# Performance work log

Measured on AMD Instinct MI355X. Metric: run time of the kernel, lower is better.

The kernel has to match this reference:

```python
import jax, jax.numpy as jnp
import numpy as np

B, C, H, W = 8, 3, 512, 512
EPS = 2e-4
N_ITER = 10  # n_iter_max default in TvChambolleDenoiser.forward


def setup_inputs() -> dict:
    key = jax.random.key(0)
    k1, k2 = jax.random.split(key)
    image = jax.random.normal(k1, (B, C, H, W), dtype=jnp.float32)
    # per-image denoising strength, typical TV weights
    weight = jax.random.uniform(k2, (B,), dtype=jnp.float32, minval=0.05, maxval=0.15)
    return {"image": image, "weight": weight}


def _denoise_tv_2d(img, w, eps=EPS, n_iter=N_ITER):
    """Chambolle TV denoising of a single 2D image (faithful to the torch loop)."""
    tau = 0.25  # 1 / (2 * ndim), ndim = 2
    numel = img.shape[0] * img.shape[1]

    def body(carry, i):
        pt, out, E_init, E_prev, done = carry
        # divergence of dual variable pt: dt = -pt.sum(0); dt[1:,:] += pt[0,:-1,:]; dt[:,1:] += pt[1,:,:-1]
        dt = -(pt[0] + pt[1])
        dt = dt.at[1:, :].add(pt[0, :-1, :])
        dt = dt.at[:, 1:].add(pt[1, :, :-1])
        out_new = jnp.where(i > 0, img + dt, img)
        Et = jnp.where(i > 0, jnp.sum(dt * dt), jnp.float32(0.0))
        # forward finite differences, zero-padded at the far boundary (gt stays 0 there)
        g0 = jnp.pad(out_new[1:, :] - out_new[:-1, :], ((0, 1), (0, 0)))
        g1 = jnp.pad(out_new[:, 1:] - out_new[:, :-1], ((0, 0), (0, 1)))
        s = g0 * g0 + g1 * g1
        # safe sqrt (forward value identical; avoids NaN grads at exact zeros)
        norm = jnp.sqrt(jnp.where(s > 0, s, 1.0)) * (s > 0)
        Et = (Et + w * jnp.sum(norm)) / numel
        gt = jnp.stack([g0, g1])  # [2, H, W]
        pt_new = (pt - tau * gt) / (1.0 + (tau / w) * norm)[None]
        E_init_new = jnp.where(i == 0, Et, E_init)
        converged = (i > 0) & (jnp.abs(E_prev - Et) < eps * E_init_new)
        # once converged (break in the torch loop), freeze all state
        pt = jnp.where(done, pt, pt_new)
        out = jnp.where(done, out, out_new)
        E_prev = jnp.where(done, E_prev, Et)
        E_init = jnp.where(done, E_init, E_init_new)
        done = done | converged
        return (pt, out, E_init, E_prev, done), None

    carry0 = (
        jnp.zeros((2,) + img.shape, img.dtype),  # pt
        img,                                      # out
        jnp.float32(0.0),                         # E_init
        jnp.float32(0.0),                         # E_previous
        jnp.bool_(False),                         # done
    )
    (pt, out, E_init, E_prev, done), _ = jax.lax.scan(body, carry0, jnp.arange(n_iter))
    return out


def reference(image, weight):
    b, c, h, w = image.shape
    imgs = image.reshape(b * c, h, w)          # each (batch, channel) slice denoised independently
    ws = jnp.repeat(weight, c)                 # per-batch weight shared across channels
    out = jax.vmap(_denoise_tv_2d)(imgs, ws)
    return out.reshape(b, c, h, w)
```

## Files before the change

kernel.cpp:

```cpp
#include <hip/hip_runtime.h>
#include <hip/hip_fp16.h>
#include <math.h>
#include <stdint.h>

#define HH 512
#define WW 512
#define NIMG 24
#define CCH 3
#define TAU 0.25f
#define TVEPS 2e-4f
#define NUMEL 262144.0f
#define NITER 10


__device__ __forceinline__ float2 h2f(uint32_t v) {
    __half2 h; *reinterpret_cast<uint32_t*>(&h) = v;
    return __half22float2(h);
}
__device__ __forceinline__ uint32_t f2h2(float a, float b) {
    __half2 h = __floats2half2_rn(a, b);
    return *reinterpret_cast<uint32_t*>(&h);
}
__device__ __forceinline__ void h4_to_f(uint2 hv, float* f) {
    float2 a = h2f(hv.x), b = h2f(hv.y);
    f[0] = a.x; f[1] = a.y; f[2] = b.x; f[3] = b.y;
}

__device__ __forceinline__ void block_reduce_store(float v0, float v1,
                                                   float* p0, float* p1, int tid) {
    for (int off = 32; off > 0; off >>= 1) {
        v0 += __shfl_down(v0, off, 64);
        v1 += __shfl_down(v1, off, 64);
    }
    __shared__ float sr[2][4];
    int wave = tid >> 6, lane = tid & 63;
    if (lane == 0) { sr[0][wave] = v0; sr[1][wave] = v1; }
    __syncthreads();
    if (tid == 0) {
        *p0 = (sr[0][0] + sr[0][1]) + (sr[0][2] + sr[0][3]);
        *p1 = (sr[1][0] + sr[1][1]) + (sr[1][2] + sr[1][3]);
    }
}

__device__ __forceinline__ void block_reduce_store1(float v, float* p, int tid) {
    for (int off = 32; off > 0; off >>= 1) v += __shfl_down(v, off, 64);
    __shared__ float sr[4];
    if ((tid & 63) == 0) sr[tid >> 6] = v;
    __syncthreads();
    if (tid == 0) *p = (sr[0] + sr[1]) + (sr[2] + sr[3]);
}

__global__ __launch_bounds__(256, 4) void tv_step0(
    const float* __restrict__ img, const float* __restrict__ weight,
    __half* __restrict__ imgh, uint32_t* __restrict__ ptout,
    float* __restrict__ pn)
{
    const int im = blockIdx.z;
    const int bid = blockIdx.y * 8 + blockIdx.x;
    const float w = weight[im / CCH];
    const int x0 = blockIdx.x * 64, y0 = blockIdx.y * 64;
    const float* imgI = img + (size_t)im * HH * WW;
    __half* hI = imgh + (size_t)im * HH * WW;
    uint32_t* pI = ptout + (size_t)im * HH * WW;
    __shared__ float s[65][68];
    const int tid = threadIdx.x;
    const int tx = tid & 15, ry = tid >> 4;
    const int gx = x0 + 4 * tx;

    float o[4][4];
    #pragma unroll
    for (int i = 0; i < 4; ++i) {
        int ey = ry + 16 * i, gy = y0 + ey;
        float4 v = *(const float4*)(imgI + (size_t)gy * WW + gx);
        o[i][0] = v.x; o[i][1] = v.y; o[i][2] = v.z; o[i][3] = v.w;
        *(float4*)&s[ey][4 * tx] = v;
    }
    if (tx == 15 && x0 + 64 < WW) {
        #pragma unroll
        for (int i = 0; i < 4; ++i) {
            int ey = ry + 16 * i, gy = y0 + ey;
            s[ey][64] = imgI[(size_t)gy * WW + x0 + 64];
        }
    }
    if (ry == 0 && y0 + 64 < HH) {
        *(float4*)&s[64][4 * tx] = *(const float4*)(imgI + (size_t)(y0 + 64) * WW + gx);
    }
    __syncthreads();

    float accn = 0.f;
    const float tw = TAU / w;
    #pragma unroll
    for (int i = 0; i < 4; ++i) {
        int ey = ry + 16 * i, gy = y0 + ey;
        float4 dn = *(float4*)&s[ey + 1][4 * tx];
        float rt_sh = __shfl_down(o[i][0], 1, 64);
        float rt = (tx == 15) ? s[ey][64] : rt_sh;
        float dnv[4] = {dn.x, dn.y, dn.z, dn.w};
        uint32_t pv[4];
        #pragma unroll
        for (int j = 0; j < 4; ++j) {
            float ov = o[i][j];
            float g0 = (gy < HH - 1) ? dnv[j] - ov : 0.f;
            float rn = (j < 3) ? o[i][j + 1] : rt;
            float g1 = (gx + j < WW - 1) ? rn - ov : 0.f;
            float ss2 = g0 * g0 + g1 * g1;
            float nrm = (ss2 > 0.f) ? sqrtf(ss2) : 0.f;
            accn += nrm;
            float inv = __builtin_amdgcn_rcpf(1.f + tw * nrm);
            pv[j] = f2h2(-TAU * g0 * inv, -TAU * g1 * inv);
        }
        size_t off = (size_t)gy * WW + gx;
        *(uint4*)(pI + off) = make_uint4(pv[0], pv[1], pv[2], pv[3]);
        *(uint2*)(hI + off) = make_uint2(f2h2(o[i][0], o[i][1]), f2h2(o[i][2], o[i][3]));
    }
    block_reduce_store1(accn, &pn[im * 64 + bid], tid);
}

__global__ __launch_bounds__(256, 4) void tv_stepN(
    int it,
    const __half* __restrict__ imgh, const float* __restrict__ weight,
    const uint32_t* __restrict__ pt_in, uint32_t* __restrict__ pt_out,
    float* __restrict__ sc, float* __restrict__ pd, float* __restrict__ pn)
{
    const int im = blockIdx.z;
    const int bid = blockIdx.y * 8 + blockIdx.x;
    const int tid = threadIdx.x;
    const float w = weight[im / CCH];

    __shared__ int sh_done;
    {
        const int slot = (it - 1) & 1;
        if (tid < 64) {
            float d = 0.f, n = pn[(slot * NIMG + im) * 64 + tid];
            if (it > 1) d = pd[(slot * NIMG + im) * 64 + tid];
            for (int off = 32; off > 0; off >>= 1) {
                d += __shfl_down(d, off, 64);
                n += __shfl_down(n, off, 64);
            }
            if (tid == 0) {
                float Eprev, Einit; int done, lastk;
                if (it == 1) {
                    float E0 = w * n / NUMEL;
                    Eprev = E0; Einit = E0; done = 0; lastk = 0;
                } else {
                    const float* sIn = sc + slot * 96;
                    Eprev = sIn[im]; Einit = sIn[24 + im];
                    done = ((const int*)sIn)[48 + im];
                    lastk = ((const int*)sIn)[72 + im];
                    if (!done) {
                        float Et = (d + w * n) / NUMEL;
                        if (fabsf(Eprev - Et) < TVEPS * Einit) { done = 1; lastk = it - 1; }
                        Eprev = Et;
                    }
                }
                if (bid == 0) {
                    float* sOut = sc + (it & 1) * 96;
                    sOut[im] = Eprev; sOut[24 + im] = Einit;
                    ((int*)sOut)[48 + im] = done;
                    ((int*)sOut)[72 + im] = lastk;
                }
                sh_done = done;
            }
        }
    }
    __syncthreads();
    if (sh_done) return;

    const int x0 = blockIdx.x * 64, y0 = blockIdx.y * 64;
    const __half* hI = imgh + (size_t)im * HH * WW;
    const uint32_t* pinI = pt_in + (size_t)im * HH * WW;
    uint32_t* poutI = pt_out + (size_t)im * HH * WW;
    __shared__ float s[65][68];
    const int tx = tid & 15, ry = tid >> 4;
    const int gx = x0 + 4 * tx;

    uint32_t c[4][4];
    float o[4][4], im4[4][4];

    #pragma unroll
    for (int i = 0; i < 4; ++i) {
        int ey = ry + 16 * i, gy = y0 + ey;
        size_t off = (size_t)gy * WW + gx;
        uint4 cv = *(const uint4*)(pinI + off);
        uint4 uv = make_uint4(0u, 0u, 0u, 0u);
        if (gy > 0) uv = *(const uint4*)(pinI + off - WW);
        uint32_t lf = (gx > 0) ? pinI[off - 1] : 0u;
        uint2 hv = *(const uint2*)(hI + off);
        float imv[4]; h4_to_f(hv, imv);
        c[i][0] = cv.x; c[i][1] = cv.y; c[i][2] = cv.z; c[i][3] = cv.w;
        uint32_t uu[4] = {uv.x, uv.y, uv.z, uv.w};
        uint32_t lt[4] = {lf, cv.x, cv.y, cv.z};
        #pragma unroll
        for (int j = 0; j < 4; ++j) {
            float2 cf = h2f(c[i][j]);
            float dt = -(cf.x + cf.y) + h2f(uu[j]).x + h2f(lt[j]).y;
            o[i][j] = imv[j] + dt;
            im4[i][j] = imv[j];
        }
        *(float4*)&s[ey][4 * tx] = make_float4(o[i][0], o[i][1], o[i][2], o[i][3]);
    }
    if (tx == 15 && x0 + 64 < WW) {
        #pragma unroll
        for (int i = 0; i < 4; ++i) {
            int ey = ry + 16 * i, gy = y0 + ey;
            size_t off = (size_t)gy * WW + x0 + 64;
            uint32_t c2 = pinI[off];
            uint32_t u2 = (gy > 0) ? pinI[off - WW] : 0u;
            float2 cf = h2f(c2);
            float dt = -(cf.x + cf.y) + h2f(u2).x + h2f(c[i][3]).y;
            s[ey][64] = __half2float(hI[off]) + dt;
        }
    }
    if (ry == 0 && y0 + 64 < HH) {
        int gy = y0 + 64;
        size_t off = (size_t)gy * WW + gx;
        uint4 cv = *(const uint4*)(pinI + off);
        uint4 uv = *(const uint4*)(pinI + off - WW);
        uint32_t lf = (gx > 0) ? pinI[off - 1] : 0u;
        uint2 hv = *(const uint2*)(hI + off);
        float imv[4]; h4_to_f(hv, imv);
        uint32_t cc[4] = {cv.x, cv.y, cv.z, cv.w};
        uint32_t uu[4] = {uv.x, uv.y, uv.z, uv.w};
        uint32_t lt[4] = {lf, cv.x, cv.y, cv.z};
        float ob[4];
        #pragma unroll
        for (int j = 0; j < 4; ++j) {
            float2 cf = h2f(cc[j]);
            ob[j] = imv[j] + (-(cf.x + cf.y) + h2f(uu[j]).x + h2f(lt[j]).y);
        }
        *(float4*)&s[64][4 * tx] = make_float4(ob[0], ob[1], ob[2], ob[3]);
    }
    __syncthreads();

    float accd = 0.f, accn = 0.f;
    const float tw = TAU / w;
    #pragma unroll
    for (int i = 0; i < 4; ++i) {
        int ey = ry + 16 * i, gy = y0 + ey;
        float4 dn = *(float4*)&s[ey + 1][4 * tx];
        float rt_sh = __shfl_down(o[i][0], 1, 64);
        float rt = (tx == 15) ? s[ey][64] : rt_sh;
        float dnv[4] = {dn.x, dn.y, dn.z, dn.w};
        uint32_t pv[4];
        #pragma unroll
        for (int j = 0; j < 4; ++j) {
            float ov = o[i][j];
            float g0 = (gy < HH - 1) ? dnv[j] - ov : 0.f;
            float rn = (j < 3) ? o[i][j + 1] : rt;
            float g1 = (gx + j < WW - 1) ? rn - ov : 0.f;
            float ss2 = g0 * g0 + g1 * g1;
            float nrm = (ss2 > 0.f) ? sqrtf(ss2) : 0.f;
            accn += nrm;
            float dt = ov - im4[i][j];
            accd += dt * dt;
            float inv = __builtin_amdgcn_rcpf(1.f + tw * nrm);
            float2 cf = h2f(c[i][j]);
            pv[j] = f2h2((cf.x - TAU * g0) * inv, (cf.y - TAU * g1) * inv);
        }
        *(uint4*)(poutI + (size_t)gy * WW + gx) = make_uint4(pv[0], pv[1], pv[2], pv[3]);
    }
    block_reduce_store(accd, accn,
                       &pd[((it & 1) * NIMG + im) * 64 + bid],
                       &pn[((it & 1) * NIMG + im) * 64 + bid], tid);
}

__global__ __launch_bounds__(256, 4) void tv_out(
    const float* __restrict__ img, float* __restrict__ out,
    const uint32_t* __restrict__ ptA, const uint32_t* __restrict__ ptB,
    const float* __restrict__ weight, const float* __restrict__ sc,
    const float* __restrict__ pd, const float* __restrict__ pn)
{
    const int im = blockIdx.z;
    const int tid = threadIdx.x;
    const float w = weight[im / CCH];
    __shared__ int2 shk;
    if (tid < 64) {
        const float* sIn = sc;
        int done = ((const int*)sIn)[48 + im];
        int lastk = ((const int*)sIn)[72 + im];
        if (!done) {
            float d = pd[im * 64 + tid];
            float n = pn[im * 64 + tid];
            for (int off = 32; off > 0; off >>= 1) {
                d += __shfl_down(d, off, 64);
                n += __shfl_down(n, off, 64);
            }
            if (tid == 0) {
                float Et = (d + w * n) / NUMEL;
                if (fabsf(sIn[im] - Et) < TVEPS * sIn[24 + im]) { done = 1; lastk = 8; }
            }
        }
        if (tid == 0) { shk.x = done; shk.y = lastk; }
    }
    __syncthreads();
    int k = shk.x ? shk.y : (NITER - 1);
    const uint32_t* p = ((((k - 1) & 1) == 0) ? ptA : ptB) + (size_t)im * HH * WW;
    const float* imgI = img + (size_t)im * HH * WW;
    float* outI = out + (size_t)im * HH * WW;
    const int x0 = blockIdx.x * 64, y0 = blockIdx.y * 64;
    const int tx = tid & 15, ry = tid >> 4;
    const int gx = x0 + 4 * tx;
    #pragma unroll
    for (int i = 0; i < 4; ++i) {
        int gy = y0 + ry + 16 * i;
        size_t off = (size_t)gy * WW + gx;
        uint4 cv = *(const uint4*)(p + off);
        uint4 uv = make_uint4(0u, 0u, 0u, 0u);
        if (gy > 0) uv = *(const uint4*)(p + off - WW);
        uint32_t lf = (gx > 0) ? p[off - 1] : 0u;
        float4 iv = *(const float4*)(imgI + off);
        uint32_t cc[4] = {cv.x, cv.y, cv.z, cv.w};
        uint32_t uu[4] = {uv.x, uv.y, uv.z, uv.w};
        uint32_t lt[4] = {lf, cv.x, cv.y, cv.z};
        float ivv[4] = {iv.x, iv.y, iv.z, iv.w};
        float r[4];
        #pragma unroll
        for (int j = 0; j < 4; ++j) {
            float2 cf = h2f(cc[j]);
            r[j] = ivv[j] + (-(cf.x + cf.y) + h2f(uu[j]).x + h2f(lt[j]).y);
        }
        *(float4*)(outI + off) = make_float4(r[0], r[1], r[2], r[3]);
    }
}

extern "C" void kernel_launch(void* const* d_in, const int* in_sizes, int n_in,
                              void* d_out, int out_size, void* d_ws, size_t ws_size,
                              hipStream_t stream)
{
    const float* img = (const float*)d_in[0];
    const float* weight = (const float*)d_in[1];
    float* out = (float*)d_out;
    float* sc = (float*)d_ws;
    float* pd = (float*)((char*)d_ws + 4096);
    float* pn = (float*)((char*)d_ws + 16384);
    __half* imgh = (__half*)((char*)d_ws + 32768);
    uint32_t* ptA = (uint32_t*)((char*)d_ws + 12615680);
    uint32_t* ptB = (uint32_t*)((char*)d_ws + 37781504);

    dim3 grid(8, 8, NIMG);
    dim3 block(256);

    tv_step0<<<grid, block, 0, stream>>>(img, weight, imgh, ptA, pn);

    for (int it = 1; it <= 8; ++it) {
        uint32_t* pin  = (((it - 1) & 1) == 0) ? ptA : ptB;
        uint32_t* pout = ((it & 1) == 0) ? ptA : ptB;
        tv_stepN<<<grid, block, 0, stream>>>(it, imgh, weight, pin, pout, sc, pd, pn);
    }
    tv_out<<<grid, block, 0, stream>>>(img, out, ptA, ptB, weight, sc, pd, pn);
}
```

Before: 262.0 us.

## Fuse two Chambolle iterations per launch using haloed shared-memory tiles

Replaces the eight per-iteration launches with four launches, each running two TV iterations on a 64x64 tile staged with a 2-pixel halo in shared memory. Halo cells are recomputed redundantly. This halves global reads and writes of the dual field and the number of kernel launches. Convergence checks now handle two energy values per launch, and the output kernel recomputes one extra step when the stopping iteration is even. In exchange it uses more LDS per block (lower occupancy bound of 3), adds redundant halo compute and several extra block barriers.

New measurement: 280.2 us. +6.9%, slower.

```diff
diff --git a/kernel.cpp b/kernel.cpp
--- a/kernel.cpp
+++ b/kernel.cpp
@@ -10,7 +10,9 @@
 #define TAU 0.25f
 #define TVEPS 2e-4f
 #define NUMEL 262144.0f
-#define NITER 10
+
+#define LSF 69
+#define LSH 70
 
 
 __device__ __forceinline__ float2 h2f(uint32_t v) {
@@ -26,34 +28,158 @@
     f[0] = a.x; f[1] = a.y; f[2] = b.x; f[3] = b.y;
 }
 
-__device__ __forceinline__ void block_reduce_store(float v0, float v1,
-                                                   float* p0, float* p1, int tid) {
+struct Smem {
+    uint32_t PT[68 * LSF];
+    float    OA[68 * LSF];
+    __half   IM[68 * LSH];
+};
+
+__device__ __forceinline__ int SUMIX(int slot, int arr, int im) {
+    return ((slot * 4 + arr) * NIMG + im) * 64;
+}
+
+__device__ void stage_pt_im(Smem& S, const uint32_t* __restrict__ ptg,
+                            const __half* __restrict__ hI,
+                            int x0, int y0, int tid) {
+    for (int idx = tid; idx < 68 * 34; idx += 256) {
+        int r = idx / 34, mq = idx - r * 34;
+        int c = 2 * mq;
+        int y = y0 - 2 + r, x = x0 - 2 + c;
+        uint2 pv = make_uint2(0u, 0u);
+        uint32_t iv = 0u;
+        if ((unsigned)y < (unsigned)HH && (unsigned)x < (unsigned)WW) {
+            size_t off = (size_t)y * WW + x;
+            pv = *(const uint2*)(ptg + off);
+            iv = *(const uint32_t*)(hI + off);
+        }
+        S.PT[r * LSF + c] = pv.x;
+        S.PT[r * LSF + c + 1] = pv.y;
+        *(uint32_t*)&S.IM[r * LSH + c] = iv;
+    }
+}
+
+template <bool ACC>
+__device__ float phase_outA(Smem& S, int tid) {
+    float acc = 0.f;
+    for (int idx = tid; idx < 67 * 67; idx += 256) {
+        int r = idx / 67, c = idx - r * 67;
+        r += 1; c += 1;
+        float2 cf = h2f(S.PT[r * LSF + c]);
+        float up = h2f(S.PT[(r - 1) * LSF + c]).x;
+        float lf = h2f(S.PT[r * LSF + c - 1]).y;
+        float im = __half2float(S.IM[r * LSH + c]);
+        float oa = im + (-(cf.x + cf.y) + up + lf);
+        S.OA[r * LSF + c] = oa;
+        if (ACC) {
+            if (r >= 2 && r < 66 && c >= 2 && c < 66) {
+                float d = oa - im;
+                acc += d * d;
+            }
+        }
+    }
+    return acc;
+}
+
+template <bool ACC>
+__device__ float phase_ptA(Smem& S, int x0, int y0, int tid, float tw) {
+    float acc = 0.f;
+    for (int idx = tid; idx < 66 * 66; idx += 256) {
+        int r = idx / 66, c = idx - r * 66;
+        r += 1; c += 1;
+        int y = y0 - 2 + r, x = x0 - 2 + c;
+        if ((unsigned)y < (unsigned)HH && (unsigned)x < (unsigned)WW) {
+            float o = S.OA[r * LSF + c];
+            float g0 = (y < HH - 1) ? S.OA[(r + 1) * LSF + c] - o : 0.f;
+            float g1 = (x < WW - 1) ? S.OA[r * LSF + c + 1] - o : 0.f;
+            float ss2 = g0 * g0 + g1 * g1;
+            float nrm = (ss2 > 0.f) ? sqrtf(ss2) : 0.f;
+            if (ACC) {
+                if (r >= 2 && r < 66 && c >= 2 && c < 66) acc += nrm;
+            }
+            float inv = __builtin_amdgcn_rcpf(1.f + tw * nrm);
+            float2 cf = h2f(S.PT[r * LSF + c]);
+            S.PT[r * LSF + c] = f2h2((cf.x - TAU * g0) * inv, (cf.y - TAU * g1) * inv);
+        } else {
+            S.PT[r * LSF + c] = 0u;
+        }
+    }
+    return acc;
+}
+
+template <bool ACC>
+__device__ float phase_outB(Smem& S, int tid) {
+    float acc = 0.f;
+    for (int idx = tid; idx < 65 * 65; idx += 256) {
+        int r = idx / 65, c = idx - r * 65;
+        r += 2; c += 2;
+        float2 cf = h2f(S.PT[r * LSF + c]);
+        float im = __half2float(S.IM[r * LSH + c]);
+        float ob = im + (-(cf.x + cf.y) + h2f(S.PT[(r - 1) * LSF + c]).x
+                         + h2f(S.PT[r * LSF + c - 1]).y);
+        S.OA[r * LSF + c] = ob;
+        if (ACC) {
+            if (r < 66 && c < 66) {
+                float d = ob - im;
+                acc += d * d;
+            }
+        }
+    }
+    return acc;
+}
+
+__device__ float phase_ptB_store(Smem& S, uint32_t* __restrict__ poutI,
+                                 int x0, int y0, int tid, float tw) {
+    const int tx = tid & 15, ry = tid >> 4;
+    const int gxb = x0 + 4 * tx;
+    float acc = 0.f;
+    #pragma unroll
+    for (int i = 0; i < 4; ++i) {
+        int gy = y0 + ry + 16 * i;
+        int r = 2 + ry + 16 * i;
+        uint32_t pv[4];
+        #pragma unroll
+        for (int j = 0; j < 4; ++j) {
+            int c = 2 + 4 * tx + j;
+            float o = S.OA[r * LSF + c];
+            float g0 = (gy < HH - 1) ? S.OA[(r + 1) * LSF + c] - o : 0.f;
+            float g1 = (gxb + j < WW - 1) ? S.OA[r * LSF + c + 1] - o : 0.f;
+            float ss2 = g0 * g0 + g1 * g1;
+            float nrm = (ss2 > 0.f) ? sqrtf(ss2) : 0.f;
+            acc += nrm;
+            float inv = __builtin_amdgcn_rcpf(1.f + tw * nrm);
+            float2 cf = h2f(S.PT[r * LSF + c]);
+            pv[j] = f2h2((cf.x - TAU * g0) * inv, (cf.y - TAU * g1) * inv);
+        }
+        *(uint4*)(poutI + (size_t)gy * WW + gxb) = make_uint4(pv[0], pv[1], pv[2], pv[3]);
+    }
+    return acc;
+}
+
+__device__ __forceinline__ void red4_store(float a, float b, float c, float d,
+                                           float* pa, float* pb, float* pc, float* pdd,
+                                           int tid) {
     for (int off = 32; off > 0; off >>= 1) {
-        v0 += __shfl_down(v0, off, 64);
-        v1 += __shfl_down(v1, off, 64);
-    }
-    __shared__ float sr[2][4];
+        a += __shfl_down(a, off, 64);
+        b += __shfl_down(b, off, 64);
+        c += __shfl_down(c, off, 64);
+        d += __shfl_down(d, off, 64);
+    }
+    __shared__ float sr[4][4];
     int wave = tid >> 6, lane = tid & 63;
-    if (lane == 0) { sr[0][wave] = v0; sr[1][wave] = v1; }
+    if (lane == 0) { sr[0][wave] = a; sr[1][wave] = b; sr[2][wave] = c; sr[3][wave] = d; }
     __syncthreads();
     if (tid == 0) {
-        *p0 = (sr[0][0] + sr[0][1]) + (sr[0][2] + sr[0][3]);
-        *p1 = (sr[1][0] + sr[1][1]) + (sr[1][2] + sr[1][3]);
-    }
-}
-
-__device__ __forceinline__ void block_reduce_store1(float v, float* p, int tid) {
-    for (int off = 32; off > 0; off >>= 1) v += __shfl_down(v, off, 64);
-    __shared__ float sr[4];
-    if ((tid & 63) == 0) sr[tid >> 6] = v;
-    __syncthreads();
-    if (tid == 0) *p = (sr[0] + sr[1]) + (sr[2] + sr[3]);
+        *pa = (sr[0][0] + sr[0][1]) + (sr[0][2] + sr[0][3]);
+        *pb = (sr[1][0] + sr[1][1]) + (sr[1][2] + sr[1][3]);
+        *pc = (sr[2][0] + sr[2][1]) + (sr[2][2] + sr[2][3]);
+        *pdd = (sr[3][0] + sr[3][1]) + (sr[3][2] + sr[3][3]);
+    }
 }
 
 __global__ __launch_bounds__(256, 4) void tv_step0(
     const float* __restrict__ img, const float* __restrict__ weight,
     __half* __restrict__ imgh, uint32_t* __restrict__ ptout,
-    float* __restrict__ pn)
+    float* __restrict__ pn0)
 {
     const int im = blockIdx.z;
     const int bid = blockIdx.y * 8 + blockIdx.x;
@@ -113,14 +239,18 @@
         *(uint4*)(pI + off) = make_uint4(pv[0], pv[1], pv[2], pv[3]);
         *(uint2*)(hI + off) = make_uint2(f2h2(o[i][0], o[i][1]), f2h2(o[i][2], o[i][3]));
     }
-    block_reduce_store1(accn, &pn[im * 64 + bid], tid);
-}
-
-__global__ __launch_bounds__(256, 4) void tv_stepN(
-    int it,
+    for (int off = 32; off > 0; off >>= 1) accn += __shfl_down(accn, off, 64);
+    __shared__ float sr[4];
+    if ((tid & 63) == 0) sr[tid >> 6] = accn;
+    __syncthreads();
+    if (tid == 0) pn0[im * 64 + bid] = (sr[0] + sr[1]) + (sr[2] + sr[3]);
+}
+
+__global__ __launch_bounds__(256, 3) void tv_fused(
+    int m,
     const __half* __restrict__ imgh, const float* __restrict__ weight,
     const uint32_t* __restrict__ pt_in, uint32_t* __restrict__ pt_out,
-    float* __restrict__ sc, float* __restrict__ pd, float* __restrict__ pn)
+    float* __restrict__ sc, float* __restrict__ sums)
 {
     const int im = blockIdx.z;
     const int bid = blockIdx.y * 8 + blockIdx.x;
@@ -129,35 +259,49 @@
 
     __shared__ int sh_done;
     {
-        const int slot = (it - 1) & 1;
+        const int sIn = (m - 1) & 1;
         if (tid < 64) {
-            float d = 0.f, n = pn[(slot * NIMG + im) * 64 + tid];
-            if (it > 1) d = pd[(slot * NIMG + im) * 64 + tid];
+            float da = 0.f, na = 0.f, db = 0.f, nb = 0.f;
+            if (m == 1) {
+                na = sums[SUMIX(0, 1, im) + tid];
+            } else {
+                da = sums[SUMIX(sIn, 0, im) + tid];
+                na = sums[SUMIX(sIn, 1, im) + tid];
+                db = sums[SUMIX(sIn, 2, im) + tid];
+                nb = sums[SUMIX(sIn, 3, im) + tid];
+            }
             for (int off = 32; off > 0; off >>= 1) {
-                d += __shfl_down(d, off, 64);
-                n += __shfl_down(n, off, 64);
+                da += __shfl_down(da, off, 64);
+                na += __shfl_down(na, off, 64);
+                db += __shfl_down(db, off, 64);
+                nb += __shfl_down(nb, off, 64);
             }
             if (tid == 0) {
                 float Eprev, Einit; int done, lastk;
-                if (it == 1) {
-                    float E0 = w * n / NUMEL;
+                if (m == 1) {
+                    float E0 = w * na / NUMEL;
                     Eprev = E0; Einit = E0; done = 0; lastk = 0;
                 } else {
-                    const float* sIn = sc + slot * 96;
-                    Eprev = sIn[im]; Einit = sIn[24 + im];
-                    done = ((const int*)sIn)[48 + im];
-                    lastk = ((const int*)sIn)[72 + im];
+                    const float* sI = sc + sIn * 128;
+                    Eprev = sI[im]; Einit = sI[32 + im];
+                    done = ((const int*)sI)[64 + im];
+                    lastk = ((const int*)sI)[96 + im];
                     if (!done) {
-                        float Et = (d + w * n) / NUMEL;
-                        if (fabsf(Eprev - Et) < TVEPS * Einit) { done = 1; lastk = it - 1; }
-                        Eprev = Et;
+                        float Et = (da + w * na) / NUMEL;
+                        if (fabsf(Eprev - Et) < TVEPS * Einit) { done = 1; lastk = 2 * m - 3; }
+                        else {
+                            Eprev = Et;
+                            Et = (db + w * nb) / NUMEL;
+                            if (fabsf(Eprev - Et) < TVEPS * Einit) { done = 1; lastk = 2 * m - 2; }
+                            else Eprev = Et;
+                        }
                     }
                 }
                 if (bid == 0) {
-                    float* sOut = sc + (it & 1) * 96;
-                    sOut[im] = Eprev; sOut[24 + im] = Einit;
-                    ((int*)sOut)[48 + im] = done;
-                    ((int*)sOut)[72 + im] = lastk;
+                    float* sO = sc + (m & 1) * 128;
+                    sO[im] = Eprev; sO[32 + im] = Einit;
+                    ((int*)sO)[64 + im] = done;
+                    ((int*)sO)[96 + im] = lastk;
                 }
                 sh_done = done;
             }
@@ -167,159 +311,128 @@
     if (sh_done) return;
 
     const int x0 = blockIdx.x * 64, y0 = blockIdx.y * 64;
-    const __half* hI = imgh + (size_t)im * HH * WW;
+    const float tw = TAU / w;
     const uint32_t* pinI = pt_in + (size_t)im * HH * WW;
     uint32_t* poutI = pt_out + (size_t)im * HH * WW;
-    __shared__ float s[65][68];
-    const int tx = tid & 15, ry = tid >> 4;
-    const int gx = x0 + 4 * tx;
-
-    uint32_t c[4][4];
-    float o[4][4], im4[4][4];
-
-    #pragma unroll
-    for (int i = 0; i < 4; ++i) {
-        int ey = ry + 16 * i, gy = y0 + ey;
-        size_t off = (size_t)gy * WW + gx;
-        uint4 cv = *(const uint4*)(pinI + off);
-        uint4 uv = make_uint4(0u, 0u, 0u, 0u);
-        if (gy > 0) uv = *(const uint4*)(pinI + off - WW);
-        uint32_t lf = (gx > 0) ? pinI[off - 1] : 0u;
-        uint2 hv = *(const uint2*)(hI + off);
-        float imv[4]; h4_to_f(hv, imv);
-        c[i][0] = cv.x; c[i][1] = cv.y; c[i][2] = cv.z; c[i][3] = cv.w;
-        uint32_t uu[4] = {uv.x, uv.y, uv.z, uv.w};
-        uint32_t lt[4] = {lf, cv.x, cv.y, cv.z};
-        #pragma unroll
-        for (int j = 0; j < 4; ++j) {
-            float2 cf = h2f(c[i][j]);
-            float dt = -(cf.x + cf.y) + h2f(uu[j]).x + h2f(lt[j]).y;
-            o[i][j] = imv[j] + dt;
-            im4[i][j] = imv[j];
-        }
-        *(float4*)&s[ey][4 * tx] = make_float4(o[i][0], o[i][1], o[i][2], o[i][3]);
-    }
-    if (tx == 15 && x0 + 64 < WW) {
-        #pragma unroll
-        for (int i = 0; i < 4; ++i) {
-            int ey = ry + 16 * i, gy = y0 + ey;
-            size_t off = (size_t)gy * WW + x0 + 64;
-            uint32_t c2 = pinI[off];
-            uint32_t u2 = (gy > 0) ? pinI[off - WW] : 0u;
-            float2 cf = h2f(c2);
-            float dt = -(cf.x + cf.y) + h2f(u2).x + h2f(c[i][3]).y;
-            s[ey][64] = __half2float(hI[off]) + dt;
-        }
-    }
-    if (ry == 0 && y0 + 64 < HH) {
-        int gy = y0 + 64;
-        size_t off = (size_t)gy * WW + gx;
-        uint4 cv = *(const uint4*)(pinI + off);
-        uint4 uv = *(const uint4*)(pinI + off - WW);
-        uint32_t lf = (gx > 0) ? pinI[off - 1] : 0u;
-        uint2 hv = *(const uint2*)(hI + off);
-        float imv[4]; h4_to_f(hv, imv);
-        uint32_t cc[4] = {cv.x, cv.y, cv.z, cv.w};
-        uint32_t uu[4] = {uv.x, uv.y, uv.z, uv.w};
-        uint32_t lt[4] = {lf, cv.x, cv.y, cv.z};
-        float ob[4];
-        #pragma unroll
-        for (int j = 0; j < 4; ++j) {
-            float2 cf = h2f(cc[j]);
-            ob[j] = imv[j] + (-(cf.x + cf.y) + h2f(uu[j]).x + h2f(lt[j]).y);
-        }
-        *(float4*)&s[64][4 * tx] = make_float4(ob[0], ob[1], ob[2], ob[3]);
-    }
-    __syncthreads();
-
-    float accd = 0.f, accn = 0.f;
-    const float tw = TAU / w;
-    #pragma unroll
-    for (int i = 0; i < 4; ++i) {
-        int ey = ry + 16 * i, gy = y0 + ey;
-        float4 dn = *(float4*)&s[ey + 1][4 * tx];
-        float rt_sh = __shfl_down(o[i][0], 1, 64);
-        float rt = (tx == 15) ? s[ey][64] : rt_sh;
-        float dnv[4] = {dn.x, dn.y, dn.z, dn.w};
-        uint32_t pv[4];
-        #pragma unroll
-        for (int j = 0; j < 4; ++j) {
-            float ov = o[i][j];
-            float g0 = (gy < HH - 1) ? dnv[j] - ov : 0.f;
-            float rn = (j < 3) ? o[i][j + 1] : rt;
-            float g1 = (gx + j < WW - 1) ? rn - ov : 0.f;
-            float ss2 = g0 * g0 + g1 * g1;
-            float nrm = (ss2 > 0.f) ? sqrtf(ss2) : 0.f;
-            accn += nrm;
-            float dt = ov - im4[i][j];
-            accd += dt * dt;
-            float inv = __builtin_amdgcn_rcpf(1.f + tw * nrm);
-            float2 cf = h2f(c[i][j]);
-            pv[j] = f2h2((cf.x - TAU * g0) * inv, (cf.y - TAU * g1) * inv);
-        }
-        *(uint4*)(poutI + (size_t)gy * WW + gx) = make_uint4(pv[0], pv[1], pv[2], pv[3]);
-    }
-    block_reduce_store(accd, accn,
-                       &pd[((it & 1) * NIMG + im) * 64 + bid],
-                       &pn[((it & 1) * NIMG + im) * 64 + bid], tid);
-}
-
-__global__ __launch_bounds__(256, 4) void tv_out(
+    const __half* hI = imgh + (size_t)im * HH * WW;
+
+    __shared__ Smem S;
+    stage_pt_im(S, pinI, hI, x0, y0, tid);
+    __syncthreads();
+    float a_d = phase_outA<true>(S, tid);
+    __syncthreads();
+    float a_n = phase_ptA<true>(S, x0, y0, tid, tw);
+    __syncthreads();
+    float b_d = phase_outB<true>(S, tid);
+    __syncthreads();
+    float b_n = phase_ptB_store(S, poutI, x0, y0, tid, tw);
+
+    const int sOut = m & 1;
+    red4_store(a_d, a_n, b_d, b_n,
+               &sums[SUMIX(sOut, 0, im) + bid], &sums[SUMIX(sOut, 1, im) + bid],
+               &sums[SUMIX(sOut, 2, im) + bid], &sums[SUMIX(sOut, 3, im) + bid], tid);
+}
+
+__global__ __launch_bounds__(256, 3) void tv_out(
     const float* __restrict__ img, float* __restrict__ out,
     const uint32_t* __restrict__ ptA, const uint32_t* __restrict__ ptB,
-    const float* __restrict__ weight, const float* __restrict__ sc,
-    const float* __restrict__ pd, const float* __restrict__ pn)
+    const __half* __restrict__ imgh, const float* __restrict__ weight,
+    const float* __restrict__ sc, const float* __restrict__ sums)
 {
     const int im = blockIdx.z;
     const int tid = threadIdx.x;
     const float w = weight[im / CCH];
+
     __shared__ int2 shk;
-    if (tid < 64) {
-        const float* sIn = sc;
-        int done = ((const int*)sIn)[48 + im];
-        int lastk = ((const int*)sIn)[72 + im];
-        if (!done) {
-            float d = pd[im * 64 + tid];
-            float n = pn[im * 64 + tid];
+    {
+        const float* sI = sc;
+        int done = ((const int*)sI)[64 + im];
+        int lastk = ((const int*)sI)[96 + im];
+        if (!done && tid < 64) {
+            float da = sums[SUMIX(0, 0, im) + tid];
+            float na = sums[SUMIX(0, 1, im) + tid];
+            float db = sums[SUMIX(0, 2, im) + tid];
+            float nb = sums[SUMIX(0, 3, im) + tid];
             for (int off = 32; off > 0; off >>= 1) {
-                d += __shfl_down(d, off, 64);
-                n += __shfl_down(n, off, 64);
+                da += __shfl_down(da, off, 64);
+                na += __shfl_down(na, off, 64);
+                db += __shfl_down(db, off, 64);
+                nb += __shfl_down(nb, off, 64);
             }
             if (tid == 0) {
-                float Et = (d + w * n) / NUMEL;
-                if (fabsf(sIn[im] - Et) < TVEPS * sIn[24 + im]) { done = 1; lastk = 8; }
+                float Eprev = sI[im], Einit = sI[32 + im];
+                float Et = (da + w * na) / NUMEL;
+                if (fabsf(Eprev - Et) < TVEPS * Einit) { done = 1; lastk = 7; }
+                else {
+                    Eprev = Et;
+                    Et = (db + w * nb) / NUMEL;
+                    if (fabsf(Eprev - Et) < TVEPS * Einit) { done = 1; lastk = 8; }
+                }
             }
         }
         if (tid == 0) { shk.x = done; shk.y = lastk; }
     }
     __syncthreads();
-    int k = shk.x ? shk.y : (NITER - 1);
-    const uint32_t* p = ((((k - 1) & 1) == 0) ? ptA : ptB) + (size_t)im * HH * WW;
+    const int k = shk.x ? shk.y : 9;
+
     const float* imgI = img + (size_t)im * HH * WW;
     float* outI = out + (size_t)im * HH * WW;
     const int x0 = blockIdx.x * 64, y0 = blockIdx.y * 64;
     const int tx = tid & 15, ry = tid >> 4;
     const int gx = x0 + 4 * tx;
-    #pragma unroll
-    for (int i = 0; i < 4; ++i) {
-        int gy = y0 + ry + 16 * i;
-        size_t off = (size_t)gy * WW + gx;
-        uint4 cv = *(const uint4*)(p + off);
-        uint4 uv = make_uint4(0u, 0u, 0u, 0u);
-        if (gy > 0) uv = *(const uint4*)(p + off - WW);
-        uint32_t lf = (gx > 0) ? p[off - 1] : 0u;
-        float4 iv = *(const float4*)(imgI + off);
-        uint32_t cc[4] = {cv.x, cv.y, cv.z, cv.w};
-        uint32_t uu[4] = {uv.x, uv.y, uv.z, uv.w};
-        uint32_t lt[4] = {lf, cv.x, cv.y, cv.z};
-        float ivv[4] = {iv.x, iv.y, iv.z, iv.w};
-        float r[4];
+
+    if (k & 1) {
+        const uint32_t* p = ((((k - 1) >> 1) & 1) ? ptB : ptA) + (size_t)im * HH * WW;
         #pragma unroll
-        for (int j = 0; j < 4; ++j) {
-            float2 cf = h2f(cc[j]);
-            r[j] = ivv[j] + (-(cf.x + cf.y) + h2f(uu[j]).x + h2f(lt[j]).y);
-        }
-        *(float4*)(outI + off) = make_float4(r[0], r[1], r[2], r[3]);
+        for (int i = 0; i < 4; ++i) {
+            int gy = y0 + ry + 16 * i;
+            size_t off = (size_t)gy * WW + gx;
+            uint4 cv = *(const uint4*)(p + off);
+            uint4 uv = make_uint4(0u, 0u, 0u, 0u);
+            if (gy > 0) uv = *(const uint4*)(p + off - WW);
+            uint32_t lf = (gx > 0) ? p[off - 1] : 0u;
+            float4 iv = *(const float4*)(imgI + off);
+            uint32_t cc[4] = {cv.x, cv.y, cv.z, cv.w};
+            uint32_t uu[4] = {uv.x, uv.y, uv.z, uv.w};
+            uint32_t lt[4] = {lf, cv.x, cv.y, cv.z};
+            float ivv[4] = {iv.x, iv.y, iv.z, iv.w};
+            float r[4];
+            #pragma unroll
+            for (int j = 0; j < 4; ++j) {
+                float2 cf = h2f(cc[j]);
+                r[j] = ivv[j] + (-(cf.x + cf.y) + h2f(uu[j]).x + h2f(lt[j]).y);
+            }
+            *(float4*)(outI + off) = make_float4(r[0], r[1], r[2], r[3]);
+        }
+    } else {
+        const uint32_t* p = ((((k - 2) >> 1) & 1) ? ptB : ptA) + (size_t)im * HH * WW;
+        const __half* hI = imgh + (size_t)im * HH * WW;
+        const float tw = TAU / w;
+        __shared__ Smem S;
+        stage_pt_im(S, p, hI, x0, y0, tid);
+        __syncthreads();
+        phase_outA<false>(S, tid);
+        __syncthreads();
+        phase_ptA<false>(S, x0, y0, tid, tw);
+        __syncthreads();
+        #pragma unroll
+        for (int i = 0; i < 4; ++i) {
+            int gy = y0 + ry + 16 * i;
+            int r = 2 + ry + 16 * i;
+            size_t off = (size_t)gy * WW + gx;
+            float4 iv = *(const float4*)(imgI + off);
+            float ivv[4] = {iv.x, iv.y, iv.z, iv.w};
+            float rr[4];
+            #pragma unroll
+            for (int j = 0; j < 4; ++j) {
+                int c = 2 + 4 * tx + j;
+                float2 cf = h2f(S.PT[r * LSF + c]);
+                float up = h2f(S.PT[(r - 1) * LSF + c]).x;
+                float lf = h2f(S.PT[r * LSF + c - 1]).y;
+                rr[j] = ivv[j] + (-(cf.x + cf.y) + up + lf);
+            }
+            *(float4*)(outI + off) = make_float4(rr[0], rr[1], rr[2], rr[3]);
+        }
     }
 }
 
@@ -331,21 +444,22 @@
     const float* weight = (const float*)d_in[1];
     float* out = (float*)d_out;
     float* sc = (float*)d_ws;
-    float* pd = (float*)((char*)d_ws + 4096);
-    float* pn = (float*)((char*)d_ws + 16384);
-    __half* imgh = (__half*)((char*)d_ws + 32768);
-    uint32_t* ptA = (uint32_t*)((char*)d_ws + 12615680);
-    uint32_t* ptB = (uint32_t*)((char*)d_ws + 37781504);
+    float* sums = (float*)((char*)d_ws + 4096);
+    __half* imgh = (__half*)((char*)d_ws + 65536);
+    uint32_t* ptA = (uint32_t*)((char*)d_ws + 12648448);
+    uint32_t* ptB = (uint32_t*)((char*)d_ws + 37814272);
 
     dim3 grid(8, 8, NIMG);
     dim3 block(256);
 
-    tv_step0<<<grid, block, 0, stream>>>(img, weight, imgh, ptA, pn);
-
-    for (int it = 1; it <= 8; ++it) {
-        uint32_t* pin  = (((it - 1) & 1) == 0) ? ptA : ptB;
-        uint32_t* pout = ((it & 1) == 0) ? ptA : ptB;
-        tv_stepN<<<grid, block, 0, stream>>>(it, imgh, weight, pin, pout, sc, pd, pn);
-    }
-    tv_out<<<grid, block, 0, stream>>>(img, out, ptA, ptB, weight, sc, pd, pn);
-}
+    tv_step0<<<grid, block, 0, stream>>>(img, weight, imgh, ptA,
+                                         sums + (0 * 4 + 1) * NIMG * 64);
+
+    for (int m = 1; m <= 4; ++m) {
+        uint32_t* pin  = (m & 1) ? ptA : ptB;
+        uint32_t* pout = (m & 1) ? ptB : ptA;
+        tv_fused<<<grid, block, 0, stream>>>(m, imgh, weight, pin, pout, sc, sums);
+    }
+
+    tv_out<<<grid, block, 0, stream>>>(img, out, ptA, ptB, imgh, weight, sc, sums);
+}
```

## Give each thread a 4x4 register tile and share halos via shuffles and LDS

Applied to the files above, without the earlier changes.

The step kernel used to give each thread four rows strided 16 apart. It now gives each thread a contiguous 4x4 patch, so the up and down neighbours mostly come from registers. Left neighbours come from wave shuffles, and only the patch boundary rows pass through small LDS arrays. This replaces the redundant per-row up and left global loads and the large 65x68 float shared tile. The divergence energy is also accumulated directly as dv*dv instead of recomputing out minus img. The cost is more edge-case logic, an extra barrier, and higher register pressure.

Measured after the change: 232.7 us. 11.2% less time.

```diff
diff --git a/kernel.cpp b/kernel.cpp
--- a/kernel.cpp
+++ b/kernel.cpp
@@ -170,95 +170,142 @@
     const __half* hI = imgh + (size_t)im * HH * WW;
     const uint32_t* pinI = pt_in + (size_t)im * HH * WW;
     uint32_t* poutI = pt_out + (size_t)im * HH * WW;
-    __shared__ float s[65][68];
-    const int tx = tid & 15, ry = tid >> 4;
+    const int tx = tid & 15, ty = tid >> 4;
     const int gx = x0 + 4 * tx;
-
-    uint32_t c[4][4];
-    float o[4][4], im4[4][4];
-
-    #pragma unroll
-    for (int i = 0; i < 4; ++i) {
-        int ey = ry + 16 * i, gy = y0 + ey;
-        size_t off = (size_t)gy * WW + gx;
-        uint4 cv = *(const uint4*)(pinI + off);
-        uint4 uv = make_uint4(0u, 0u, 0u, 0u);
-        if (gy > 0) uv = *(const uint4*)(pinI + off - WW);
-        uint32_t lf = (gx > 0) ? pinI[off - 1] : 0u;
-        uint2 hv = *(const uint2*)(hI + off);
-        float imv[4]; h4_to_f(hv, imv);
-        c[i][0] = cv.x; c[i][1] = cv.y; c[i][2] = cv.z; c[i][3] = cv.w;
-        uint32_t uu[4] = {uv.x, uv.y, uv.z, uv.w};
-        uint32_t lt[4] = {lf, cv.x, cv.y, cv.z};
+    const int gy0 = y0 + 4 * ty;
+    const float tw = TAU / w;
+
+    __shared__ uint4  XP[16][16];
+    __shared__ float4 XO[16][16];
+
+    uint4 c[4]; uint2 ih[4];
+    #pragma unroll
+    for (int i = 0; i < 4; ++i) {
+        size_t off = (size_t)(gy0 + i) * WW + gx;
+        c[i] = *(const uint4*)(pinI + off);
+        ih[i] = *(const uint2*)(hI + off);
+    }
+    XP[ty][tx] = c[3];
+
+    uint32_t lf[4] = {0u, 0u, 0u, 0u};
+    if (tx == 0 && x0 > 0) {
+        #pragma unroll
+        for (int i = 0; i < 4; ++i) lf[i] = pinI[(size_t)(gy0 + i) * WW + x0 - 1];
+    }
+    uint4 upg = make_uint4(0u, 0u, 0u, 0u);
+    if (ty == 0 && y0 > 0) upg = *(const uint4*)(pinI + (size_t)(y0 - 1) * WW + gx);
+
+    uint32_t ep[5] = {0u, 0u, 0u, 0u, 0u};
+    float ihE[4] = {0.f, 0.f, 0.f, 0.f};
+    const bool hasE = (tx == 15) && (x0 + 64 < WW);
+    if (hasE) {
+        const int xe = x0 + 64;
+        ep[0] = (gy0 > 0) ? pinI[(size_t)(gy0 - 1) * WW + xe] : 0u;
+        #pragma unroll
+        for (int i = 0; i < 4; ++i) {
+            ep[i + 1] = pinI[(size_t)(gy0 + i) * WW + xe];
+            ihE[i] = __half2float(hI[(size_t)(gy0 + i) * WW + xe]);
+        }
+    }
+    uint4 sp = make_uint4(0u, 0u, 0u, 0u); uint2 ihS = make_uint2(0u, 0u);
+    uint32_t spl = 0u;
+    const bool hasS = (ty == 15) && (y0 + 64 < HH);
+    if (hasS) {
+        size_t off = (size_t)(y0 + 64) * WW + gx;
+        sp = *(const uint4*)(pinI + off);
+        ihS = *(const uint2*)(hI + off);
+        if (tx == 0 && x0 > 0) spl = pinI[(size_t)(y0 + 64) * WW + x0 - 1];
+    }
+    __syncthreads();
+
+    uint4 up4 = (ty > 0) ? XP[ty - 1][tx] : upg;
+    float o[4][4];
+    float accd = 0.f;
+    {
+        uint32_t ca[4][4] = {{c[0].x, c[0].y, c[0].z, c[0].w},
+                             {c[1].x, c[1].y, c[1].z, c[1].w},
+                             {c[2].x, c[2].y, c[2].z, c[2].w},
+                             {c[3].x, c[3].y, c[3].z, c[3].w}};
+        uint32_t ua[4] = {up4.x, up4.y, up4.z, up4.w};
+        #pragma unroll
+        for (int i = 0; i < 4; ++i) {
+            uint32_t lsh = __shfl_up(ca[i][3], 1, 64);
+            uint32_t lw = (tx > 0) ? lsh : lf[i];
+            float imv[4]; h4_to_f(ih[i], imv);
+            #pragma unroll
+            for (int j = 0; j < 4; ++j) {
+                float2 cf = h2f(ca[i][j]);
+                float up = (i > 0) ? h2f(ca[i - 1][j]).x : h2f(ua[j]).x;
+                float le = (j > 0) ? h2f(ca[i][j - 1]).y : h2f(lw).y;
+                float dv = -(cf.x + cf.y) + up + le;
+                o[i][j] = imv[j] + dv;
+                accd += dv * dv;
+            }
+        }
+    }
+
+    float he[4] = {0.f, 0.f, 0.f, 0.f};
+    if (hasE) {
+        uint32_t prev = ep[0];
+        #pragma unroll
+        for (int i = 0; i < 4; ++i) {
+            float2 cf = h2f(ep[i + 1]);
+            float up = h2f(prev).x;
+            float le = h2f(c[i].w).y;
+            he[i] = ihE[i] + (-(cf.x + cf.y) + up + le);
+            prev = ep[i + 1];
+        }
+    }
+    float hs[4] = {0.f, 0.f, 0.f, 0.f};
+    if (hasS) {
+        uint32_t ssh = __shfl_up(sp.w, 1, 64);
+        uint32_t sl = (tx > 0) ? ssh : spl;
+        uint32_t sa[4] = {sp.x, sp.y, sp.z, sp.w};
+        float smv[4]; h4_to_f(ihS, smv);
         #pragma unroll
         for (int j = 0; j < 4; ++j) {
-            float2 cf = h2f(c[i][j]);
-            float dt = -(cf.x + cf.y) + h2f(uu[j]).x + h2f(lt[j]).y;
-            o[i][j] = imv[j] + dt;
-            im4[i][j] = imv[j];
-        }
-        *(float4*)&s[ey][4 * tx] = make_float4(o[i][0], o[i][1], o[i][2], o[i][3]);
-    }
-    if (tx == 15 && x0 + 64 < WW) {
-        #pragma unroll
-        for (int i = 0; i < 4; ++i) {
-            int ey = ry + 16 * i, gy = y0 + ey;
-            size_t off = (size_t)gy * WW + x0 + 64;
-            uint32_t c2 = pinI[off];
-            uint32_t u2 = (gy > 0) ? pinI[off - WW] : 0u;
-            float2 cf = h2f(c2);
-            float dt = -(cf.x + cf.y) + h2f(u2).x + h2f(c[i][3]).y;
-            s[ey][64] = __half2float(hI[off]) + dt;
-        }
-    }
-    if (ry == 0 && y0 + 64 < HH) {
-        int gy = y0 + 64;
-        size_t off = (size_t)gy * WW + gx;
-        uint4 cv = *(const uint4*)(pinI + off);
-        uint4 uv = *(const uint4*)(pinI + off - WW);
-        uint32_t lf = (gx > 0) ? pinI[off - 1] : 0u;
-        uint2 hv = *(const uint2*)(hI + off);
-        float imv[4]; h4_to_f(hv, imv);
-        uint32_t cc[4] = {cv.x, cv.y, cv.z, cv.w};
-        uint32_t uu[4] = {uv.x, uv.y, uv.z, uv.w};
-        uint32_t lt[4] = {lf, cv.x, cv.y, cv.z};
-        float ob[4];
-        #pragma unroll
-        for (int j = 0; j < 4; ++j) {
-            float2 cf = h2f(cc[j]);
-            ob[j] = imv[j] + (-(cf.x + cf.y) + h2f(uu[j]).x + h2f(lt[j]).y);
-        }
-        *(float4*)&s[64][4 * tx] = make_float4(ob[0], ob[1], ob[2], ob[3]);
-    }
-    __syncthreads();
-
-    float accd = 0.f, accn = 0.f;
-    const float tw = TAU / w;
-    #pragma unroll
-    for (int i = 0; i < 4; ++i) {
-        int ey = ry + 16 * i, gy = y0 + ey;
-        float4 dn = *(float4*)&s[ey + 1][4 * tx];
-        float rt_sh = __shfl_down(o[i][0], 1, 64);
-        float rt = (tx == 15) ? s[ey][64] : rt_sh;
-        float dnv[4] = {dn.x, dn.y, dn.z, dn.w};
+            float2 cf = h2f(sa[j]);
+            float up = h2f(c[3].x * 0u + (&c[3].x)[j]).x;
+            float le = (j > 0) ? h2f(sa[j - 1]).y : h2f(sl).y;
+            hs[j] = smv[j] + (-(cf.x + cf.y) + up + le);
+        }
+    }
+
+    XO[ty][tx] = make_float4(o[0][0], o[0][1], o[0][2], o[0][3]);
+    __syncthreads();
+
+    float bel4[4];
+    if (ty < 15) {
+        float4 t = XO[ty + 1][tx];
+        bel4[0] = t.x; bel4[1] = t.y; bel4[2] = t.z; bel4[3] = t.w;
+    } else {
+        bel4[0] = hs[0]; bel4[1] = hs[1]; bel4[2] = hs[2]; bel4[3] = hs[3];
+    }
+    float accn = 0.f;
+    #pragma unroll
+    for (int i = 0; i < 4; ++i) {
+        int gy = gy0 + i;
+        float esh = __shfl_down(o[i][0], 1, 64);
+        float rt = (tx < 15) ? esh : he[i];
+        uint32_t ca[4] = {c[i].x, c[i].y, c[i].z, c[i].w};
         uint32_t pv[4];
         #pragma unroll
         for (int j = 0; j < 4; ++j) {
             float ov = o[i][j];
-            float g0 = (gy < HH - 1) ? dnv[j] - ov : 0.f;
+            float below = (i < 3) ? o[i + 1][j] : bel4[j];
+            float g0 = (gy < HH - 1) ? below - ov : 0.f;
             float rn = (j < 3) ? o[i][j + 1] : rt;
             float g1 = (gx + j < WW - 1) ? rn - ov : 0.f;
             float ss2 = g0 * g0 + g1 * g1;
             float nrm = (ss2 > 0.f) ? sqrtf(ss2) : 0.f;
             accn += nrm;
-            float dt = ov - im4[i][j];
-            accd += dt * dt;
             float inv = __builtin_amdgcn_rcpf(1.f + tw * nrm);
-            float2 cf = h2f(c[i][j]);
+            float2 cf = h2f(ca[j]);
             pv[j] = f2h2((cf.x - TAU * g0) * inv, (cf.y - TAU * g1) * inv);
         }
         *(uint4*)(poutI + (size_t)gy * WW + gx) = make_uint4(pv[0], pv[1], pv[2], pv[3]);
     }
+
     block_reduce_store(accd, accn,
                        &pd[((it & 1) * NIMG + im) * 64 + bid],
                        &pn[((it & 1) * NIMG + im) * 64 + bid], tid);
@@ -307,11 +354,11 @@
         uint4 cv = *(const uint4*)(p + off);
         uint4 uv = make_uint4(0u, 0u, 0u, 0u);
         if (gy > 0) uv = *(const uint4*)(p + off - WW);
-        uint32_t lf = (gx > 0) ? p[off - 1] : 0u;
+        uint32_t lfv = (gx > 0) ? p[off - 1] : 0u;
         float4 iv = *(const float4*)(imgI + off);
         uint32_t cc[4] = {cv.x, cv.y, cv.z, cv.w};
         uint32_t uu[4] = {uv.x, uv.y, uv.z, uv.w};
-        uint32_t lt[4] = {lf, cv.x, cv.y, cv.z};
+        uint32_t lt[4] = {lfv, cv.x, cv.y, cv.z};
         float ivv[4] = {iv.x, iv.y, iv.z, iv.w};
         float r[4];
         #pragma unroll
@@ -341,7 +388,6 @@
     dim3 block(256);
 
     tv_step0<<<grid, block, 0, stream>>>(img, weight, imgh, ptA, pn);
-
     for (int it = 1; it <= 8; ++it) {
         uint32_t* pin  = (((it - 1) & 1) == 0) ? ptA : ptB;
         uint32_t* pout = ((it & 1) == 0) ? ptA : ptB;
```
